# Performance work log

Measured on AMD Instinct MI355X. Metric: run time of the kernel, lower is better.

Reference implementation:

```python
import jax, jax.numpy as jnp
import numpy as np

B, C, H, W = 32, 512, 32, 32
K, D = 1024, 512  # codebook_size, latent_dim


def setup_inputs() -> dict:
    key = jax.random.key(0)
    k1, k2 = jax.random.split(key)
    z = jax.random.normal(k1, (B, C, H, W), dtype=jnp.float32)
    # nn.Embedding weight init: uniform(-1/codebook_size, 1/codebook_size)
    codebook = jax.random.uniform(k2, (K, D), dtype=jnp.float32,
                                  minval=-1.0 / K, maxval=1.0 / K)
    return {"z": z, "codebook": codebook}


def reference(z, codebook):
    b, c, h, w = z.shape
    # [B, C, H, W] -> [B, H, W, C] -> [B*H*W, C]
    z_flat = jnp.transpose(z, (0, 2, 3, 1)).reshape(-1, c)
    # squared euclidean distances via ||z||^2 - 2 z.W^T + ||W||^2
    distances = (
        jnp.sum(z_flat * z_flat, axis=1, keepdims=True)
        - 2.0 * jnp.matmul(z_flat, codebook.T)
        + jnp.sum(codebook * codebook, axis=1)[None, :]
    )  # [B*H*W, K]
    min_indices = jnp.argmin(distances, axis=1)  # [B*H*W]
    # Faithful to the original: gather then reshape directly to z.shape
    # (no inverse permute), which works because C == latent_dim.
    quantized = codebook[min_indices].reshape(z.shape)
    return quantized, min_indices.reshape(b, -1)
```

## Files before the change

kernel.cpp:

```cpp
#include <hip/hip_runtime.h>
#include <hip/hip_bf16.h>

#define M_ROWS  32768
#define D_DIM   512
#define K_CODES 1024
#define HW      1024
#define IMG_STRIDE (D_DIM * HW)

#define WH_OFF   0u
#define A_OFF    1048576u
#define W_OFF    1179648u
#define PK_OFF   1183744u
#define PART_OFF 1312768u
#define WL1_OFF  3934208u
#define WL2_OFF  4065280u
#define CNT_OFF  4196352u

#define WINDOW 5.0e-4f

__device__ __forceinline__ float fmul32(float a, float b) {
  float r; asm volatile("v_mul_f32 %0, %1, %2" : "=v"(r) : "v"(a), "v"(b)); return r;
}
__device__ __forceinline__ float fadd32(float a, float b) {
  float r; asm volatile("v_add_f32 %0, %1, %2" : "=v"(r) : "v"(a), "v"(b)); return r;
}
__device__ __forceinline__ float pair8(const float* r) {
  return fadd32(fadd32(fadd32(r[0], r[1]), fadd32(r[2], r[3])),
                fadd32(fadd32(r[4], r[5]), fadd32(r[6], r[7])));
}

__device__ __forceinline__ unsigned short f2bf(float x) {
  __hip_bfloat16 h = __float2bfloat16(x);
  unsigned short u; __builtin_memcpy(&u, &h, 2); return u;
}

typedef __attribute__((ext_vector_type(8))) short b8;
typedef __attribute__((ext_vector_type(4))) float f4;

struct T3 { float s1, s2, s3; int n1, n2; };
__device__ __forceinline__ void t3_merge(T3& a, const T3& bb) {
  T3 x = a, y = bb;
  bool bf = (y.s1 < x.s1) || (y.s1 == x.s1 && y.n1 < x.n1);
  if (bf) { T3 t = x; x = y; y = t; }
  float rs2; int rn2; float rs3;
  bool c2 = (y.s1 < x.s2) || (y.s1 == x.s2 && y.n1 < x.n2);
  if (c2) { rs2 = y.s1; rn2 = y.n1; rs3 = fminf(x.s2, y.s2); }
  else    { rs2 = x.s2; rn2 = x.n2; rs3 = fminf(x.s3, y.s1); }
  a.s1 = x.s1; a.n1 = x.n1; a.s2 = rs2; a.n2 = rn2; a.s3 = rs3;
}

__global__ __launch_bounds__(128) void vq_prep(const float* __restrict__ z,
                                               float* __restrict__ A,
                                               char* __restrict__ zh_b) {
  __shared__ float zs[2][64 * 68];
  const int wave = threadIdx.x >> 6, t = threadIdx.x & 63;
  const int i0 = blockIdx.x * 128 + wave * 64;
  const int b = i0 >> 10, hw0 = i0 & 1023;
  const float* zbase = z + (size_t)b * IMG_STRIDE + hw0;
  float* zsw = zs[wave];
  const int pos = i0 + t;
  const size_t mbase = (size_t)(pos >> 4) * 1024 + (size_t)(pos & 15) * 16;
  float r8[8], blk[4];
  alignas(16) unsigned short hs[8];
#pragma unroll
  for (int ch = 0; ch < 8; ++ch) {
    __syncthreads();
    {
      const int l = t & 15, j0 = t >> 4;
#pragma unroll
      for (int jj = 0; jj < 16; ++jj) {
        int j = j0 * 16 + jj;
        float4 vv = *(const float4*)(zbase + (size_t)(ch * 64 + j) * HW + 4 * l);
        *(float4*)(zsw + j * 68 + 4 * l) = vv;
      }
    }
    __syncthreads();
#pragma unroll
    for (int j = 0; j < 64; ++j) {
      const int c = ch * 64 + j;
      float v = zsw[j * 68 + t];
      hs[j & 7] = f2bf(v);
      if ((j & 7) == 7) {
        const int kc = c >> 5, q = (c >> 3) & 3;
        *(uint4*)(zh_b + (size_t)kc * 2097152 + q * 256 + mbase) = *(uint4*)hs;
      }
      float pq = fmul32(v, v);
      const int k = c & 7, m = c & 127;
      if (m < 8) r8[k] = pq;
      else       r8[k] = fadd32(r8[k], pq);
      if (m == 127) blk[c >> 7] = pair8(r8);
    }
  }
  A[pos] = fadd32(fadd32(blk[0], blk[1]), fadd32(blk[2], blk[3]));
}

__global__ void vq_prepw(const float* __restrict__ cb, float* __restrict__ W,
                         char* __restrict__ wh_b, int* __restrict__ cnt) {
  if (blockIdx.x == 0 && threadIdx.x < 2) cnt[threadIdx.x] = 0;
  const int n = blockIdx.x * 256 + threadIdx.x;
  const float* wp = cb + (size_t)n * D_DIM;
  const size_t nbase = (size_t)(n >> 4) * 1024 + (size_t)(n & 15) * 16;
  float r8[8], blk[4];
  alignas(16) unsigned short hs[8];
#pragma unroll
  for (int bb = 0; bb < 4; ++bb) {
#pragma unroll
    for (int g = 0; g < 16; ++g) {
      float vv[8];
#pragma unroll
      for (int k = 0; k < 8; ++k) vv[k] = wp[bb * 128 + g * 8 + k];
#pragma unroll
      for (int k = 0; k < 8; ++k) {
        float pq = fmul32(vv[k], vv[k]);
        if (g == 0) r8[k] = pq;
        else        r8[k] = fadd32(r8[k], pq);
        hs[k] = f2bf(vv[k]);
      }
      const int kc = bb * 4 + (g >> 2), q = g & 3;
      *(uint4*)(wh_b + (size_t)kc * 65536 + q * 256 + nbase) = *(uint4*)hs;
    }
    blk[bb] = pair8(r8);
  }
  W[n] = fadd32(fadd32(blk[0], blk[1]), fadd32(blk[2], blk[3]));
}

__global__ __launch_bounds__(256, 2) void vq_score(
    const char* __restrict__ zh_b, const char* __restrict__ wh_b,
    const float* __restrict__ Wws, float* __restrict__ part)
{
  __shared__ float red[1280];
  const int tid = threadIdx.x;
  const int lane = tid & 63, wave = tid >> 6;
  const int wr = wave >> 1, wc = wave & 1;
  const int bm = blockIdx.x & 255, bn = blockIdx.x >> 8;
  const int m0 = bm * 128, n0 = bn * 256;

  f4 acc[4][8];
#pragma unroll
  for (int r = 0; r < 4; ++r)
#pragma unroll
    for (int v = 0; v < 8; ++v) acc[r][v] = (f4)(0.0f);

  const char* gA_w = zh_b + (size_t)bm * 8192 + (size_t)(wr * 4) * 1024 + (size_t)lane * 16;
  const char* gB_w = wh_b + (size_t)bn * 16384 + (size_t)(wc * 8) * 1024 + (size_t)lane * 16;

  b8 ar[2][4], br[2][8];
#pragma unroll
  for (int r = 0; r < 4; ++r)
    ar[0][r] = *(const b8*)(gA_w + (size_t)r * 1024);
#pragma unroll
  for (int v = 0; v < 8; ++v)
    br[0][v] = *(const b8*)(gB_w + (size_t)v * 1024);

#pragma unroll
  for (int kc = 0; kc < 16; ++kc) {
    const int cur = kc & 1, nxt = cur ^ 1;
    if (kc + 1 < 16) {
      const char* gA = gA_w + (size_t)(kc + 1) * 2097152;
      const char* gB = gB_w + (size_t)(kc + 1) * 65536;
#pragma unroll
      for (int r = 0; r < 4; ++r) ar[nxt][r] = *(const b8*)(gA + (size_t)r * 1024);
#pragma unroll
      for (int v = 0; v < 8; ++v) br[nxt][v] = *(const b8*)(gB + (size_t)v * 1024);
    }
#pragma unroll
    for (int r = 0; r < 4; ++r) {
#pragma unroll
      for (int v = 0; v < 8; ++v)
        acc[r][v] = __builtin_amdgcn_mfma_f32_16x16x32_bf16(ar[cur][r], br[cur][v],
                                                            acc[r][v], 0, 0, 0);
    }
  }

  const int l15 = lane & 15, quad = lane >> 4;
  float sW[8];
#pragma unroll
  for (int v = 0; v < 8; ++v) sW[v] = Wws[n0 + wc * 128 + v * 16 + l15];

#pragma unroll
  for (int r = 0; r < 4; ++r) {
#pragma unroll
    for (int reg = 0; reg < 4; ++reg) {
      T3 t; t.s1 = t.s2 = t.s3 = 3.4e38f; t.n1 = 0; t.n2 = 0;
#pragma unroll
      for (int v = 0; v < 8; ++v) {
        float s = fmaf(-2.f, acc[r][v][reg], sW[v]);
        int n = n0 + wc * 128 + v * 16 + l15;
        if (s < t.s1)      { t.s3 = t.s2; t.s2 = t.s1; t.n2 = t.n1; t.s1 = s; t.n1 = n; }
        else if (s < t.s2) { t.s3 = t.s2; t.s2 = s; t.n2 = n; }
        else if (s < t.s3) { t.s3 = s; }
      }
#pragma unroll
      for (int m = 1; m <= 8; m <<= 1) {
        T3 o;
        o.s1 = __shfl_xor(t.s1, m); o.s2 = __shfl_xor(t.s2, m); o.s3 = __shfl_xor(t.s3, m);
        o.n1 = __shfl_xor(t.n1, m); o.n2 = __shfl_xor(t.n2, m);
        t3_merge(t, o);
      }
      if (l15 == 0) {
        int row = wr * 64 + r * 16 + quad * 4 + reg;
        float* d = red + (row * 2 + wc) * 5;
        d[0] = t.s1; d[1] = t.s2; d[2] = t.s3; d[3] = (float)t.n1; d[4] = (float)t.n2;
      }
    }
  }
  __syncthreads();
  if (tid < 128) {
    const float* d0 = red + (tid * 2) * 5;
    const float* d1 = red + (tid * 2 + 1) * 5;
    T3 a; a.s1 = d0[0]; a.s2 = d0[1]; a.s3 = d0[2]; a.n1 = (int)d0[3]; a.n2 = (int)d0[4];
    T3 b; b.s1 = d1[0]; b.s2 = d1[1]; b.s3 = d1[2]; b.n1 = (int)d1[3]; b.n2 = (int)d1[4];
    t3_merge(a, b);
    float* p = part + ((size_t)(m0 + tid) * 4 + bn) * 5;
    p[0] = a.s1; p[1] = a.s2; p[2] = a.s3; p[3] = (float)a.n1; p[4] = (float)a.n2;
  }
}

__global__ void vq_comb(const float* __restrict__ part, float* __restrict__ out_idx,
                        unsigned int* __restrict__ pk, int* __restrict__ wl1,
                        int* __restrict__ wl2, int* __restrict__ cnt) {
  int row = blockIdx.x * 256 + threadIdx.x;
  const float* p = part + (size_t)row * 20;
  T3 a; a.s1 = p[0]; a.s2 = p[1]; a.s3 = p[2]; a.n1 = (int)p[3]; a.n2 = (int)p[4];
#pragma unroll
  for (int j = 1; j < 4; ++j) {
    const float* q = p + j * 5;
    T3 b; b.s1 = q[0]; b.s2 = q[1]; b.s3 = q[2]; b.n1 = (int)q[3]; b.n2 = (int)q[4];
    t3_merge(a, b);
  }
  out_idx[row] = (float)a.n1;
  unsigned int f = 0;
  if (a.s2 - a.s1 < WINDOW) f = (a.s3 - a.s1 < WINDOW) ? 2u : 1u;
  pk[row] = (unsigned int)a.n1 | ((unsigned int)a.n2 << 10) | (f << 20);
  if (f == 1u) wl1[atomicAdd(&cnt[0], 1)] = row;
  if (f == 2u) wl2[atomicAdd(&cnt[1], 1)] = row;
}

__global__ __launch_bounds__(256) void vq_recheckA(
    const float* __restrict__ z, const float* __restrict__ cb,
    const float* __restrict__ Aws, const float* __restrict__ Wws,
    const unsigned int* __restrict__ pk, float* __restrict__ out_idx)
{
  const int wave = threadIdx.x >> 6, lane = threadIdx.x & 63;
  const int row = blockIdx.x * 4 + wave;
  unsigned int p = pk[row];
  if (((p >> 20) & 3u) != 1u) return;
  int n1 = p & 1023, n2 = (p >> 10) & 1023;
  int b = row >> 10, hw = row & 1023;
  const float* zr = z + (size_t)b * IMG_STRIDE + hw;
  const float* c1p = cb + (size_t)n1 * D_DIM;
  const float* c2p = cb + (size_t)n2 * D_DIM;
  double d1 = 0.0, d2 = 0.0;
#pragma unroll
  for (int j = 0; j < 8; ++j) {
    int c = lane + 64 * j;
    double zv = (double)zr[(size_t)c * HW];
    d1 += zv * (double)c1p[c];
    d2 += zv * (double)c2p[c];
  }
#pragma unroll
  for (int off = 32; off > 0; off >>= 1) {
    d1 += __shfl_down(d1, off);
    d2 += __shfl_down(d2, off);
  }
  if (lane == 0) {
    float A_ = Aws[row];
    float e1 = fadd32(fadd32(A_, -2.f * (float)d1), Wws[n1]);
    float e2 = fadd32(fadd32(A_, -2.f * (float)d2), Wws[n2]);
    int win = (e2 < e1 || (e2 == e1 && n2 < n1)) ? n2 : n1;
    out_idx[row] = (float)win;
  }
}

__global__ __launch_bounds__(256) void vq_recheckB(
    const float* __restrict__ z, const float* __restrict__ cb,
    const float* __restrict__ Aws, const float* __restrict__ Wws,
    const int* __restrict__ wl2, const int* __restrict__ cnt,
    float* __restrict__ out_idx)
{
  __shared__ double zd[512];
  __shared__ float rd[256];
  __shared__ int rn[256];
  const int c2 = cnt[1];
  for (int t = blockIdx.x; t < c2; t += gridDim.x) {
    int row = wl2[t];
    int b = row >> 10, hw = row & 1023;
    const float* zr = z + (size_t)b * IMG_STRIDE + hw;
    for (int c = threadIdx.x; c < 512; c += 256) zd[c] = (double)zr[(size_t)c * HW];
    __syncthreads();
    float best = 3.4e38f; int bn_ = 0;
    float A_ = Aws[row];
    for (int k = 0; k < 4; ++k) {
      int n = k * 256 + threadIdx.x;
      const float* cn = cb + (size_t)n * D_DIM;
      double a0 = 0.0, a1 = 0.0, a2 = 0.0, a3 = 0.0;
#pragma unroll 8
      for (int c4 = 0; c4 < 128; ++c4) {
        float4 w4 = *(const float4*)(cn + 4 * c4);
        a0 += zd[4 * c4 + 0] * (double)w4.x;
        a1 += zd[4 * c4 + 1] * (double)w4.y;
        a2 += zd[4 * c4 + 2] * (double)w4.z;
        a3 += zd[4 * c4 + 3] * (double)w4.w;
      }
      double dot = (a0 + a1) + (a2 + a3);
      float e = fadd32(fadd32(A_, -2.f * (float)dot), Wws[n]);
      if (e < best || (e == best && n < bn_)) { best = e; bn_ = n; }
    }
    rd[threadIdx.x] = best; rn[threadIdx.x] = bn_;
    __syncthreads();
    for (int s = 128; s > 0; s >>= 1) {
      if (threadIdx.x < s) {
        float eo = rd[threadIdx.x + s]; int no = rn[threadIdx.x + s];
        if (eo < rd[threadIdx.x] || (eo == rd[threadIdx.x] && no < rn[threadIdx.x])) {
          rd[threadIdx.x] = eo; rn[threadIdx.x] = no;
        }
      }
      __syncthreads();
    }
    if (threadIdx.x == 0) out_idx[row] = (float)rn[0];
    __syncthreads();
  }
}

__global__ __launch_bounds__(256) void vq_gather(const float* __restrict__ cb,
                                                 const float* __restrict__ out_idx,
                                                 float* __restrict__ out_q) {
  __shared__ int bidx[16];
  const int i0 = blockIdx.x * 16;
  if (threadIdx.x < 16) bidx[threadIdx.x] = (int)out_idx[i0 + threadIdx.x];
  __syncthreads();
  float* outp = out_q + (size_t)i0 * D_DIM;
#pragma unroll
  for (int j = 0; j < 8; ++j) {
    int f4i = j * 256 + threadIdx.x;
    int row = f4i >> 7, d4 = f4i & 127;
    float4 vv = *(const float4*)(cb + (size_t)bidx[row] * D_DIM + 4 * d4);
    *(float4*)(outp + 4 * f4i) = vv;
  }
}

extern "C" void kernel_launch(void* const* d_in, const int* in_sizes, int n_in,
                              void* d_out, int out_size, void* d_ws, size_t ws_size,
                              hipStream_t stream) {
  const float* z  = (const float*)d_in[0];
  const float* cb = (const float*)d_in[1];
  float* out_q   = (float*)d_out;
  float* out_idx = (float*)d_out + (size_t)M_ROWS * D_DIM;
  char* zh_b = (char*)d_out;
  char* ws = (char*)d_ws;
  char* wh_b = ws + WH_OFF;
  float* Aws = (float*)(ws + A_OFF);
  float* Wws = (float*)(ws + W_OFF);
  unsigned int* pk = (unsigned int*)(ws + PK_OFF);
  float* part = (float*)(ws + PART_OFF);
  int* wl1 = (int*)(ws + WL1_OFF);
  int* wl2 = (int*)(ws + WL2_OFF);
  int* cnt = (int*)(ws + CNT_OFF);

  vq_prep    <<<256, 128, 0, stream>>>(z, Aws, zh_b);
  vq_prepw   <<<4, 256, 0, stream>>>(cb, Wws, wh_b, cnt);
  vq_score   <<<1024, 256, 0, stream>>>(zh_b, wh_b, Wws, part);
  vq_comb    <<<128, 256, 0, stream>>>(part, out_idx, pk, wl1, wl2, cnt);
  vq_recheckA<<<8192, 256, 0, stream>>>(z, cb, Aws, Wws, pk, out_idx);
  vq_recheckB<<<512, 256, 0, stream>>>(z, cb, Aws, Wws, wl2, cnt, out_idx);
  vq_gather  <<<2048, 256, 0, stream>>>(cb, out_idx, out_q);
}
```

Baseline: 351.1 us.

## Fuse codebook prep into z prep and merge combine, recheck, gather kernels

Codebook bf16 packing and norm computation run as extra blocks of the z prep kernel instead of a separate launch. The partial top-3 combine, the two-candidate recheck and the codebook gather are merged into one wave-per-row kernel. The full-recheck kernel now also writes its own gathered rows. This cuts kernel launches and removes the intermediate packed-index buffer and the separate gather pass. The cost is that each wave handles one row and all lanes redundantly read the partials.

```diff
diff --git a/kernel.cpp b/kernel.cpp
--- a/kernel.cpp
+++ b/kernel.cpp
@@ -51,8 +51,41 @@
 
 __global__ __launch_bounds__(128) void vq_prep(const float* __restrict__ z,
                                                float* __restrict__ A,
-                                               char* __restrict__ zh_b) {
+                                               char* __restrict__ zh_b,
+                                               const float* __restrict__ cb,
+                                               float* __restrict__ W,
+                                               char* __restrict__ wh_b,
+                                               int* __restrict__ cnt) {
   __shared__ float zs[2][64 * 68];
+  if (blockIdx.x >= 256) {
+    if (blockIdx.x == 256 && threadIdx.x < 2) cnt[threadIdx.x] = 0;
+    const int n = (blockIdx.x - 256) * 128 + threadIdx.x;
+    const float* wp = cb + (size_t)n * D_DIM;
+    const size_t nbase = (size_t)(n >> 4) * 1024 + (size_t)(n & 15) * 16;
+    float r8w[8], blkw[4];
+    alignas(16) unsigned short hsw[8];
+#pragma unroll
+    for (int bb = 0; bb < 4; ++bb) {
+#pragma unroll
+      for (int g = 0; g < 16; ++g) {
+        float vv[8];
+#pragma unroll
+        for (int k = 0; k < 8; ++k) vv[k] = wp[bb * 128 + g * 8 + k];
+#pragma unroll
+        for (int k = 0; k < 8; ++k) {
+          float pq = fmul32(vv[k], vv[k]);
+          if (g == 0) r8w[k] = pq;
+          else        r8w[k] = fadd32(r8w[k], pq);
+          hsw[k] = f2bf(vv[k]);
+        }
+        const int kc = bb * 4 + (g >> 2), q = g & 3;
+        *(uint4*)(wh_b + (size_t)kc * 65536 + q * 256 + nbase) = *(uint4*)hsw;
+      }
+      blkw[bb] = pair8(r8w);
+    }
+    W[n] = fadd32(fadd32(blkw[0], blkw[1]), fadd32(blkw[2], blkw[3]));
+    return;
+  }
   const int wave = threadIdx.x >> 6, t = threadIdx.x & 63;
   const int i0 = blockIdx.x * 128 + wave * 64;
   const int b = i0 >> 10, hw0 = i0 & 1023;
@@ -92,36 +125,6 @@
     }
   }
   A[pos] = fadd32(fadd32(blk[0], blk[1]), fadd32(blk[2], blk[3]));
-}
-
-__global__ void vq_prepw(const float* __restrict__ cb, float* __restrict__ W,
-                         char* __restrict__ wh_b, int* __restrict__ cnt) {
-  if (blockIdx.x == 0 && threadIdx.x < 2) cnt[threadIdx.x] = 0;
-  const int n = blockIdx.x * 256 + threadIdx.x;
-  const float* wp = cb + (size_t)n * D_DIM;
-  const size_t nbase = (size_t)(n >> 4) * 1024 + (size_t)(n & 15) * 16;
-  float r8[8], blk[4];
-  alignas(16) unsigned short hs[8];
-#pragma unroll
-  for (int bb = 0; bb < 4; ++bb) {
-#pragma unroll
-    for (int g = 0; g < 16; ++g) {
-      float vv[8];
-#pragma unroll
-      for (int k = 0; k < 8; ++k) vv[k] = wp[bb * 128 + g * 8 + k];
-#pragma unroll
-      for (int k = 0; k < 8; ++k) {
-        float pq = fmul32(vv[k], vv[k]);
-        if (g == 0) r8[k] = pq;
-        else        r8[k] = fadd32(r8[k], pq);
-        hs[k] = f2bf(vv[k]);
-      }
-      const int kc = bb * 4 + (g >> 2), q = g & 3;
-      *(uint4*)(wh_b + (size_t)kc * 65536 + q * 256 + nbase) = *(uint4*)hs;
-    }
-    blk[bb] = pair8(r8);
-  }
-  W[n] = fadd32(fadd32(blk[0], blk[1]), fadd32(blk[2], blk[3]));
 }
 
 __global__ __launch_bounds__(256, 2) void vq_score(
@@ -216,10 +219,14 @@
   }
 }
 
-__global__ void vq_comb(const float* __restrict__ part, float* __restrict__ out_idx,
-                        unsigned int* __restrict__ pk, int* __restrict__ wl1,
-                        int* __restrict__ wl2, int* __restrict__ cnt) {
-  int row = blockIdx.x * 256 + threadIdx.x;
+__global__ __launch_bounds__(256) void vq_final(
+    const float* __restrict__ part, const float* __restrict__ z,
+    const float* __restrict__ cb, const float* __restrict__ Aws,
+    const float* __restrict__ Wws, float* __restrict__ out_idx,
+    float* __restrict__ out_q, int* __restrict__ wl2, int* __restrict__ cnt)
+{
+  const int wave = threadIdx.x >> 6, lane = threadIdx.x & 63;
+  const int row = blockIdx.x * 4 + wave;
   const float* p = part + (size_t)row * 20;
   T3 a; a.s1 = p[0]; a.s2 = p[1]; a.s3 = p[2]; a.n1 = (int)p[3]; a.n2 = (int)p[4];
 #pragma unroll
@@ -228,55 +235,52 @@
     T3 b; b.s1 = q[0]; b.s2 = q[1]; b.s3 = q[2]; b.n1 = (int)q[3]; b.n2 = (int)q[4];
     t3_merge(a, b);
   }
-  out_idx[row] = (float)a.n1;
   unsigned int f = 0;
   if (a.s2 - a.s1 < WINDOW) f = (a.s3 - a.s1 < WINDOW) ? 2u : 1u;
-  pk[row] = (unsigned int)a.n1 | ((unsigned int)a.n2 << 10) | (f << 20);
-  if (f == 1u) wl1[atomicAdd(&cnt[0], 1)] = row;
-  if (f == 2u) wl2[atomicAdd(&cnt[1], 1)] = row;
-}
-
-__global__ __launch_bounds__(256) void vq_recheckA(
-    const float* __restrict__ z, const float* __restrict__ cb,
-    const float* __restrict__ Aws, const float* __restrict__ Wws,
-    const unsigned int* __restrict__ pk, float* __restrict__ out_idx)
-{
-  const int wave = threadIdx.x >> 6, lane = threadIdx.x & 63;
-  const int row = blockIdx.x * 4 + wave;
-  unsigned int p = pk[row];
-  if (((p >> 20) & 3u) != 1u) return;
-  int n1 = p & 1023, n2 = (p >> 10) & 1023;
-  int b = row >> 10, hw = row & 1023;
-  const float* zr = z + (size_t)b * IMG_STRIDE + hw;
-  const float* c1p = cb + (size_t)n1 * D_DIM;
-  const float* c2p = cb + (size_t)n2 * D_DIM;
-  double d1 = 0.0, d2 = 0.0;
-#pragma unroll
-  for (int j = 0; j < 8; ++j) {
-    int c = lane + 64 * j;
-    double zv = (double)zr[(size_t)c * HW];
-    d1 += zv * (double)c1p[c];
-    d2 += zv * (double)c2p[c];
-  }
-#pragma unroll
-  for (int off = 32; off > 0; off >>= 1) {
-    d1 += __shfl_down(d1, off);
-    d2 += __shfl_down(d2, off);
-  }
-  if (lane == 0) {
-    float A_ = Aws[row];
-    float e1 = fadd32(fadd32(A_, -2.f * (float)d1), Wws[n1]);
-    float e2 = fadd32(fadd32(A_, -2.f * (float)d2), Wws[n2]);
-    int win = (e2 < e1 || (e2 == e1 && n2 < n1)) ? n2 : n1;
-    out_idx[row] = (float)win;
-  }
+  if (f == 2u) {
+    if (lane == 0) wl2[atomicAdd(&cnt[1], 1)] = row;
+    return;
+  }
+  int win = a.n1;
+  if (f == 1u) {
+    int n1 = a.n1, n2 = a.n2;
+    int b = row >> 10, hw = row & 1023;
+    const float* zr = z + (size_t)b * IMG_STRIDE + hw;
+    const float* c1p = cb + (size_t)n1 * D_DIM;
+    const float* c2p = cb + (size_t)n2 * D_DIM;
+    double d1 = 0.0, d2 = 0.0;
+#pragma unroll
+    for (int j = 0; j < 8; ++j) {
+      int c = lane + 64 * j;
+      double zv = (double)zr[(size_t)c * HW];
+      d1 += zv * (double)c1p[c];
+      d2 += zv * (double)c2p[c];
+    }
+#pragma unroll
+    for (int off = 32; off > 0; off >>= 1) {
+      d1 += __shfl_down(d1, off);
+      d2 += __shfl_down(d2, off);
+    }
+    if (lane == 0) {
+      float A_ = Aws[row];
+      float e1 = fadd32(fadd32(A_, -2.f * (float)d1), Wws[n1]);
+      float e2 = fadd32(fadd32(A_, -2.f * (float)d2), Wws[n2]);
+      win = (e2 < e1 || (e2 == e1 && n2 < n1)) ? n2 : n1;
+    }
+    win = __shfl(win, 0);
+  }
+  if (lane == 0) out_idx[row] = (float)win;
+  const float4* src = (const float4*)(cb + (size_t)win * D_DIM);
+  float4* dst = (float4*)(out_q + (size_t)row * D_DIM);
+  dst[lane]      = src[lane];
+  dst[lane + 64] = src[lane + 64];
 }
 
 __global__ __launch_bounds__(256) void vq_recheckB(
     const float* __restrict__ z, const float* __restrict__ cb,
     const float* __restrict__ Aws, const float* __restrict__ Wws,
     const int* __restrict__ wl2, const int* __restrict__ cnt,
-    float* __restrict__ out_idx)
+    float* __restrict__ out_idx, float* __restrict__ out_q)
 {
   __shared__ double zd[512];
   __shared__ float rd[256];
@@ -317,25 +321,14 @@
       }
       __syncthreads();
     }
-    if (threadIdx.x == 0) out_idx[row] = (float)rn[0];
-    __syncthreads();
-  }
-}
-
-__global__ __launch_bounds__(256) void vq_gather(const float* __restrict__ cb,
-                                                 const float* __restrict__ out_idx,
-                                                 float* __restrict__ out_q) {
-  __shared__ int bidx[16];
-  const int i0 = blockIdx.x * 16;
-  if (threadIdx.x < 16) bidx[threadIdx.x] = (int)out_idx[i0 + threadIdx.x];
-  __syncthreads();
-  float* outp = out_q + (size_t)i0 * D_DIM;
-#pragma unroll
-  for (int j = 0; j < 8; ++j) {
-    int f4i = j * 256 + threadIdx.x;
-    int row = f4i >> 7, d4 = f4i & 127;
-    float4 vv = *(const float4*)(cb + (size_t)bidx[row] * D_DIM + 4 * d4);
-    *(float4*)(outp + 4 * f4i) = vv;
+    int winb = rn[0];
+    if (threadIdx.x == 0) out_idx[row] = (float)winb;
+    {
+      const float4* src = (const float4*)(cb + (size_t)winb * D_DIM);
+      float4* dst = (float4*)(out_q + (size_t)row * D_DIM);
+      if (threadIdx.x < 128) dst[threadIdx.x] = src[threadIdx.x];
+    }
+    __syncthreads();
   }
 }
 
@@ -351,17 +344,12 @@
   char* wh_b = ws + WH_OFF;
   float* Aws = (float*)(ws + A_OFF);
   float* Wws = (float*)(ws + W_OFF);
-  unsigned int* pk = (unsigned int*)(ws + PK_OFF);
   float* part = (float*)(ws + PART_OFF);
-  int* wl1 = (int*)(ws + WL1_OFF);
   int* wl2 = (int*)(ws + WL2_OFF);
   int* cnt = (int*)(ws + CNT_OFF);
 
-  vq_prep    <<<256, 128, 0, stream>>>(z, Aws, zh_b);
-  vq_prepw   <<<4, 256, 0, stream>>>(cb, Wws, wh_b, cnt);
+  vq_prep    <<<264, 128, 0, stream>>>(z, Aws, zh_b, cb, Wws, wh_b, cnt);
   vq_score   <<<1024, 256, 0, stream>>>(zh_b, wh_b, Wws, part);
-  vq_comb    <<<128, 256, 0, stream>>>(part, out_idx, pk, wl1, wl2, cnt);
-  vq_recheckA<<<8192, 256, 0, stream>>>(z, cb, Aws, Wws, pk, out_idx);
-  vq_recheckB<<<512, 256, 0, stream>>>(z, cb, Aws, Wws, wl2, cnt, out_idx);
-  vq_gather  <<<2048, 256, 0, stream>>>(cb, out_idx, out_q);
-}
+  vq_final   <<<8192, 256, 0, stream>>>(part, z, cb, Aws, Wws, out_idx, out_q, wl2, cnt);
+  vq_recheckB<<<512, 256, 0, stream>>>(z, cb, Aws, Wws, wl2, cnt, out_idx, out_q);
+}
```

Result: faster. 298.9 us (-14.9%).
